# Kernel tuning notes

Measured on AMD Instinct MI355X. Metric: run time of the kernel, lower is better.

## Reference

```python
import jax, jax.numpy as jnp
import numpy as np

B, T, D = 8, 2048, 1024


def setup_inputs() -> dict:
    key = jax.random.key(0)
    ks = jax.random.split(key, 9)
    s = 1.0 / np.sqrt(D)
    return {
        "e": jax.random.normal(ks[0], (B, T, D), jnp.float32),
        "residual": jax.random.normal(ks[1], (B, T, D), jnp.float32),
        "Wq_w": jax.random.normal(ks[2], (D, D), jnp.float32) * s,
        "Wq_b": jax.random.normal(ks[3], (D,), jnp.float32) * s,
        "Wk_w": jax.random.normal(ks[4], (D, D), jnp.float32) * s,
        "Wk_b": jax.random.normal(ks[5], (D,), jnp.float32) * s,
        "Wv_w": jax.random.normal(ks[6], (D, D), jnp.float32) * s,
        "Wv_b": jax.random.normal(ks[7], (D,), jnp.float32) * s,
        "v_table": jax.random.normal(ks[8], (T, 1), jnp.float32),
    }


def reference(e, residual, Wq_w, Wq_b, Wk_w, Wk_b, Wv_w, Wv_b, v_table):
    T_ = e.shape[1]
    # relative position index: pos[i,j] = max(i - j, 0)
    pos = jnp.arange(T_)
    rel = jnp.maximum(pos[:, None] - pos[None, :], 0)          # (T, T) int
    pos_embd = v_table[rel, 0]                                 # (T, T) gather from Embedding(length, 1)

    # torch Linear: x @ W.T + b
    Q = e @ Wq_w.T + Wq_b                                      # (B, T, D)
    K = residual @ Wk_w.T + Wk_b                               # (B, T, D)
    V = e @ Wv_w.T + Wv_b                                      # (B, T, D)

    # Q @ K^T  (torch: Q @ Wk(residual).transpose(-2,-1))
    scores = jnp.einsum('btd,bsd->bts', Q, K)                  # (B, T, T)
    # einsum('BeT,Tt->BTt', K^T, pos_embd) == sum_e K[B,T,e] * pos_embd[T,t]
    scores = scores + K.sum(-1)[:, :, None] * pos_embd[None]   # (B, T, T)

    # causal mask via tril (zeros strictly-upper entries); NO softmax in this variant
    scores = scores * jnp.tril(jnp.ones((T_, T_), scores.dtype))
    return scores @ V                                          # (B, T, D)
```

## Files before the change

kernel.cpp:

```cpp
#include <hip/hip_runtime.h>

typedef unsigned short u16;
typedef __attribute__((ext_vector_type(8))) short bf16x8;
typedef __attribute__((ext_vector_type(8))) unsigned short u16x8;
typedef __attribute__((ext_vector_type(4))) float f32x4;

static __device__ __forceinline__ u16 f2bf(float f) {
  unsigned u = __float_as_uint(f);
  u += 0x7FFFu + ((u >> 16) & 1u);
  return (u16)(u >> 16);
}
static __device__ __forceinline__ float bf2f(u16 h) {
  return __uint_as_float(((unsigned)h) << 16);
}

__global__ __launch_bounds__(256) void conv_big(const float* __restrict__ e,
                                                const float* __restrict__ res,
                                                u16* __restrict__ eb, u16* __restrict__ rb) {
  int i = blockIdx.x * 256 + threadIdx.x;
  const float* in = blockIdx.z ? res : e;
  u16* out = blockIdx.z ? rb : eb;
  const float4* p = (const float4*)in + (size_t)i * 2;
  float4 a = p[0], b = p[1];
  u16x8 r;
  r[0] = f2bf(a.x); r[1] = f2bf(a.y); r[2] = f2bf(a.z); r[3] = f2bf(a.w);
  r[4] = f2bf(b.x); r[5] = f2bf(b.y); r[6] = f2bf(b.z); r[7] = f2bf(b.w);
  ((u16x8*)out)[i] = r;
}
__global__ __launch_bounds__(256) void conv_w(const float* __restrict__ w0,
                                              const float* __restrict__ w1,
                                              const float* __restrict__ w2,
                                              u16* __restrict__ o0, u16* __restrict__ o1,
                                              u16* __restrict__ o2) {
  int i = blockIdx.x * 256 + threadIdx.x;
  const float* in = blockIdx.z == 0 ? w0 : (blockIdx.z == 1 ? w1 : w2);
  u16* out = blockIdx.z == 0 ? o0 : (blockIdx.z == 1 ? o1 : o2);
  const float4* p = (const float4*)in + (size_t)i * 2;
  float4 a = p[0], b = p[1];
  u16x8 r;
  r[0] = f2bf(a.x); r[1] = f2bf(a.y); r[2] = f2bf(a.z); r[3] = f2bf(a.w);
  r[4] = f2bf(b.x); r[5] = f2bf(b.y); r[6] = f2bf(b.z); r[7] = f2bf(b.w);
  ((u16x8*)out)[i] = r;
}

__global__ __launch_bounds__(256) void ksum_kernel(const u16* __restrict__ K,
                                                   float* __restrict__ out) {
  int row = blockIdx.x * 4 + (threadIdx.x >> 6);
  int lane = threadIdx.x & 63;
  const u16x8* p = (const u16x8*)(K + (size_t)row * 1024);
  float s = 0.f;
#pragma unroll
  for (int it = 0; it < 2; ++it) {
    u16x8 v = p[lane + it * 64];
#pragma unroll
    for (int j = 0; j < 8; ++j) s += bf2f(v[j]);
  }
#pragma unroll
  for (int off = 32; off >= 1; off >>= 1) s += __shfl_down(s, off);
  if (lane == 0) out[row] = s;
}

enum { M_BIASN = 0, M_BIASM = 1, M_SCORES = 2, M_OUT = 3 };

template <int MODE, int SWZ>
static __device__ __forceinline__ void core256x128(
    const u16* __restrict__ Ab, int lda, const u16* __restrict__ Bb, int ldb,
    char* smem, int m0, int n0, int nk, void* __restrict__ Cbase, int ldc,
    const float* __restrict__ bias, const float* __restrict__ ksb,
    const float* __restrict__ vtab) {
  const int tid = threadIdx.x;
  const int lane = tid & 63;
  const int wid = tid >> 6;
  const int wm = wid >> 1, wn = wid & 1;

  char* As = smem;
  char* Bs = smem + 32768;

  const int r7 = (tid >> 3) & 7;
  const int cb = (tid & 7) << 4;
  const int gcol = SWZ ? (cb ^ (r7 << 4)) : cb;
  const int rbase_st = tid >> 3;

  const int aoff = (wm * 64 + (lane & 15)) * 128;
  const int boff = (wn * 64 + (lane & 15)) * 128;
  const int swz7 = SWZ ? (lane & 7) : 0;
  const int c0 = ((0 * 4 + (lane >> 4)) ^ swz7) << 4;
  const int c1 = ((1 * 4 + (lane >> 4)) ^ swz7) << 4;

  f32x4 acc[4][4];
#pragma unroll
  for (int m = 0; m < 4; ++m)
#pragma unroll
    for (int n = 0; n < 4; ++n) acc[m][n] = (f32x4){0.f, 0.f, 0.f, 0.f};

  for (int kt = 0; kt < nk; ++kt) {
    const int k0 = kt * 64;
#pragma unroll
    for (int i = 0; i < 4; ++i) {
      const char* ga = (const char*)(Ab + (size_t)(m0 + i * 64 + rbase_st) * lda + k0) + gcol;
      __builtin_amdgcn_global_load_lds(
          (const __attribute__((address_space(1))) void*)ga,
          (__attribute__((address_space(3))) void*)(As + i * 8192 + wid * 1024), 16, 0, 0);
    }
#pragma unroll
    for (int j = 0; j < 2; ++j) {
      const char* gb = (const char*)(Bb + (size_t)(n0 + j * 64 + rbase_st) * ldb + k0) + gcol;
      __builtin_amdgcn_global_load_lds(
          (const __attribute__((address_space(1))) void*)gb,
          (__attribute__((address_space(3))) void*)(Bs + j * 8192 + wid * 1024), 16, 0, 0);
    }
    __syncthreads();
#pragma unroll
    for (int ks = 0; ks < 2; ++ks) {
      const int cks = ks ? c1 : c0;
      bf16x8 af[4], bfv[4];
#pragma unroll
      for (int m = 0; m < 4; ++m) af[m] = *(const bf16x8*)(As + aoff + m * 2048 + cks);
#pragma unroll
      for (int n = 0; n < 4; ++n) bfv[n] = *(const bf16x8*)(Bs + boff + n * 2048 + cks);
#pragma unroll
      for (int m = 0; m < 4; ++m)
#pragma unroll
        for (int n = 0; n < 4; ++n)
          acc[m][n] = __builtin_amdgcn_mfma_f32_16x16x32_bf16(af[m], bfv[n], acc[m][n], 0, 0, 0);
    }
    __syncthreads();
  }

  u16* C16 = (u16*)Cbase;
  float* Cf = (float*)Cbase;
#pragma unroll
  for (int m = 0; m < 4; ++m) {
#pragma unroll
    for (int n = 0; n < 4; ++n) {
      const int rb = m0 + wm * 64 + m * 16 + ((lane >> 4) << 2);
      const int c = n0 + wn * 64 + n * 16 + (lane & 15);
#pragma unroll
      for (int j = 0; j < 4; ++j) {
        const int r = rb + j;
        float v = acc[m][n][j];
        if (MODE == M_BIASN) {
          v += bias[c];
          C16[(size_t)r * ldc + c] = f2bf(v);
        } else if (MODE == M_BIASM) {
          v += bias[r];
          C16[(size_t)r * ldc + c] = f2bf(v);
        } else if (MODE == M_SCORES) {
          if (c <= r) v += ksb[r] * vtab[r - c];
          else v = 0.f;
          C16[(size_t)r * ldc + c] = f2bf(v);
        } else {
          Cf[(size_t)r * ldc + c] = v;
        }
      }
    }
  }
}

template <int MODE, int SWZ>
static __device__ __forceinline__ void rect_gemm(
    const u16* A, int lda, long long sA, const u16* B, int ldb, long long sB,
    void* Cv, int ldc, long long sC, int k_len, const float* bias) {
  const int nl = gridDim.x * gridDim.y;
  const int l = blockIdx.x + gridDim.x * blockIdx.y;
  const int q8 = nl >> 3;
  const int logical = (l & 7) * q8 + (l >> 3);
  const int gx = logical % gridDim.x;
  const int gy = logical / gridDim.x;
  const int z = blockIdx.z;
  __shared__ char smem[49152];
  core256x128<MODE, SWZ>(A + (size_t)z * sA, lda, B + (size_t)z * sB, ldb, smem,
                         gy * 256, gx * 128, k_len >> 6,
                         (char*)Cv + 0, ldc, bias, nullptr, nullptr);
}

__global__ __launch_bounds__(512, 4) void k_q_proj(
    const u16* A, const u16* B, u16* C, const float* bias) {
  const int nl = gridDim.x * gridDim.y;
  const int l = blockIdx.x + gridDim.x * blockIdx.y;
  const int logical = (l & 7) * (nl >> 3) + (l >> 3);
  const int gx = logical % gridDim.x, gy = logical / gridDim.x;
  __shared__ char smem[49152];
  core256x128<M_BIASN, 0>(A, 1024, B, 1024, smem, gy * 256, gx * 128, 16,
                          C, 1024, bias, nullptr, nullptr);
}
__global__ __launch_bounds__(512, 4) void k_k_proj(
    const u16* A, const u16* B, u16* C, const float* bias) {
  const int nl = gridDim.x * gridDim.y;
  const int l = blockIdx.x + gridDim.x * blockIdx.y;
  const int logical = (l & 7) * (nl >> 3) + (l >> 3);
  const int gx = logical % gridDim.x, gy = logical / gridDim.x;
  __shared__ char smem[49152];
  core256x128<M_BIASN, 1>(A, 1024, B, 1024, smem, gy * 256, gx * 128, 16,
                          C, 1024, bias, nullptr, nullptr);
}
__global__ __launch_bounds__(512, 4) void k_v_proj(
    const u16* A, const u16* B, u16* C, const float* bias) {
  const int nl = gridDim.x * gridDim.y;
  const int l = blockIdx.x + gridDim.x * blockIdx.y;
  const int logical = (l & 7) * (nl >> 3) + (l >> 3);
  const int gx = logical % gridDim.x, gy = logical / gridDim.x;
  __shared__ char smem[49152];
  core256x128<M_BIASM, 1>(A, 1024, B, 1024, smem, gy * 256, gx * 128, 16,
                          C, 16384, bias, nullptr, nullptr);
}
__global__ __launch_bounds__(512, 4) void k_scores(
    const u16* Q, const u16* K, u16* S, const float* ksum, const float* vtab) {
  const int h = (blockIdx.x & 7) * 9 + (blockIdx.x >> 3);
  int gy = 0;
#pragma unroll
  for (int q = 1; q < 8; ++q) if (q * q + q <= h) gy = q;
  const int gx = h - (gy * gy + gy);
  const int z = blockIdx.z;
  __shared__ char smem[49152];
  core256x128<M_SCORES, 1>(Q + (size_t)z * 2048 * 1024, 1024,
                           K + (size_t)z * 2048 * 1024, 1024, smem,
                           gy * 256, gx * 128, 16,
                           S + (size_t)z * 2048 * 2048, 2048,
                           nullptr, ksum + (size_t)z * 2048, vtab);
}
__global__ __launch_bounds__(512, 4) void k_out(
    const u16* S, const u16* VT, float* O) {
  const int nl = gridDim.x * gridDim.y;
  const int l = blockIdx.x + gridDim.x * blockIdx.y;
  const int logical = (l & 7) * (nl >> 3) + (l >> 3);
  const int gx = logical % gridDim.x;
  const int p = logical / gridDim.x;
  const int z = blockIdx.z;
  __shared__ char smem[49152];
#pragma unroll
  for (int sub = 0; sub < 2; ++sub) {
    const int gy = sub ? 7 - p : p;
    const int nk = (gy + 1) * 4;
    core256x128<M_OUT, 1>(S + (size_t)z * 2048 * 2048, 2048,
                          VT + (size_t)z * 2048, 16384, smem,
                          gy * 256, gx * 128, nk,
                          O + (size_t)z * 2048 * 1024, 1024,
                          nullptr, nullptr, nullptr);
    if (sub == 0) __syncthreads();
  }
}

extern "C" void kernel_launch(void* const* d_in, const int* in_sizes, int n_in,
                              void* d_out, int out_size, void* d_ws, size_t ws_size,
                              hipStream_t stream) {
  (void)in_sizes; (void)n_in; (void)out_size; (void)ws_size;
  const float* e    = (const float*)d_in[0];
  const float* res  = (const float*)d_in[1];
  const float* Wq_w = (const float*)d_in[2];
  const float* Wq_b = (const float*)d_in[3];
  const float* Wk_w = (const float*)d_in[4];
  const float* Wk_b = (const float*)d_in[5];
  const float* Wv_w = (const float*)d_in[6];
  const float* Wv_b = (const float*)d_in[7];
  const float* vtab = (const float*)d_in[8];

  char* ws = (char*)d_ws;
  const size_t SZ = 33554432;
  u16* ebf = (u16*)(ws);
  u16* rbf = (u16*)(ws + SZ);
  u16* Qb  = (u16*)(ws + 2 * SZ);
  u16* Kb  = (u16*)(ws + 3 * SZ);
  u16* VT  = (u16*)(ws + 4 * SZ);
  u16* Wqb = (u16*)(ws + 5 * SZ);
  u16* Wkb = (u16*)(ws + 5 * SZ + 2097152);
  u16* Wvb = (u16*)(ws + 5 * SZ + 2 * 2097152);
  float* ksum = (float*)(ws + 5 * SZ + 3 * 2097152);
  u16* scores = (u16*)(ws);

  conv_big<<<dim3(8192, 1, 2), 256, 0, stream>>>(e, res, ebf, rbf);
  conv_w<<<dim3(512, 1, 3), 256, 0, stream>>>(Wq_w, Wk_w, Wv_w, Wqb, Wkb, Wvb);

  k_q_proj<<<dim3(8, 64, 1), 512, 0, stream>>>(ebf, Wqb, Qb, Wq_b);
  k_k_proj<<<dim3(8, 64, 1), 512, 0, stream>>>(rbf, Wkb, Kb, Wk_b);
  k_v_proj<<<dim3(128, 4, 1), 512, 0, stream>>>(Wvb, ebf, VT, Wv_b);

  ksum_kernel<<<4096, 256, 0, stream>>>(Kb, ksum);

  k_scores<<<dim3(72, 1, 8), 512, 0, stream>>>(Qb, Kb, scores, ksum, vtab);

  k_out<<<dim3(8, 4, 8), 512, 0, stream>>>(scores, VT, (float*)d_out);
}
```

Baseline: 304.4 us.

## Switch GEMMs from 256x128 to 128x128 tiles and merge Q/K projections

Replaces the 256x128 block tile (512 threads) with a 128x128 tile (256 threads) and less LDS for all GEMM kernels, and updates the triangular scheduling for scores and output to the finer 16x16 block grid. The Q and K projections are merged into one launch using the z grid dimension. The aim is finer causal-triangle granularity, so fewer masked-out tiles are computed, plus more blocks for occupancy and load balance. In exchange, data reuse per tile drops and global/LDS traffic per FLOP rises.

```diff
diff --git a/kernel.cpp b/kernel.cpp
--- a/kernel.cpp
+++ b/kernel.cpp
@@ -62,8 +62,8 @@
 
 enum { M_BIASN = 0, M_BIASM = 1, M_SCORES = 2, M_OUT = 3 };
 
-template <int MODE, int SWZ>
-static __device__ __forceinline__ void core256x128(
+template <int MODE>
+static __device__ __forceinline__ void core128(
     const u16* __restrict__ Ab, int lda, const u16* __restrict__ Bb, int ldb,
     char* smem, int m0, int n0, int nk, void* __restrict__ Cbase, int ldc,
     const float* __restrict__ bias, const float* __restrict__ ksb,
@@ -74,18 +74,15 @@
   const int wm = wid >> 1, wn = wid & 1;
 
   char* As = smem;
-  char* Bs = smem + 32768;
-
-  const int r7 = (tid >> 3) & 7;
-  const int cb = (tid & 7) << 4;
-  const int gcol = SWZ ? (cb ^ (r7 << 4)) : cb;
+  char* Bs = smem + 16384;
+
   const int rbase_st = tid >> 3;
+  const int gcol = ((tid & 7) << 4) ^ ((rbase_st & 7) << 4);
 
   const int aoff = (wm * 64 + (lane & 15)) * 128;
   const int boff = (wn * 64 + (lane & 15)) * 128;
-  const int swz7 = SWZ ? (lane & 7) : 0;
-  const int c0 = ((0 * 4 + (lane >> 4)) ^ swz7) << 4;
-  const int c1 = ((1 * 4 + (lane >> 4)) ^ swz7) << 4;
+  const int c0 = ((0 * 4 + (lane >> 4)) ^ (lane & 7)) << 4;
+  const int c1 = ((1 * 4 + (lane >> 4)) ^ (lane & 7)) << 4;
 
   f32x4 acc[4][4];
 #pragma unroll
@@ -97,17 +94,17 @@
     const int k0 = kt * 64;
 #pragma unroll
     for (int i = 0; i < 4; ++i) {
-      const char* ga = (const char*)(Ab + (size_t)(m0 + i * 64 + rbase_st) * lda + k0) + gcol;
+      const char* ga = (const char*)(Ab + (size_t)(m0 + i * 32 + rbase_st) * lda + k0) + gcol;
       __builtin_amdgcn_global_load_lds(
           (const __attribute__((address_space(1))) void*)ga,
-          (__attribute__((address_space(3))) void*)(As + i * 8192 + wid * 1024), 16, 0, 0);
-    }
-#pragma unroll
-    for (int j = 0; j < 2; ++j) {
-      const char* gb = (const char*)(Bb + (size_t)(n0 + j * 64 + rbase_st) * ldb + k0) + gcol;
+          (__attribute__((address_space(3))) void*)(As + i * 4096 + wid * 1024), 16, 0, 0);
+    }
+#pragma unroll
+    for (int i = 0; i < 4; ++i) {
+      const char* gb = (const char*)(Bb + (size_t)(n0 + i * 32 + rbase_st) * ldb + k0) + gcol;
       __builtin_amdgcn_global_load_lds(
           (const __attribute__((address_space(1))) void*)gb,
-          (__attribute__((address_space(3))) void*)(Bs + j * 8192 + wid * 1024), 16, 0, 0);
+          (__attribute__((address_space(3))) void*)(Bs + i * 4096 + wid * 1024), 16, 0, 0);
     }
     __syncthreads();
 #pragma unroll
@@ -157,86 +154,64 @@
   }
 }
 
-template <int MODE, int SWZ>
-static __device__ __forceinline__ void rect_gemm(
-    const u16* A, int lda, long long sA, const u16* B, int ldb, long long sB,
-    void* Cv, int ldc, long long sC, int k_len, const float* bias) {
-  const int nl = gridDim.x * gridDim.y;
-  const int l = blockIdx.x + gridDim.x * blockIdx.y;
-  const int q8 = nl >> 3;
-  const int logical = (l & 7) * q8 + (l >> 3);
-  const int gx = logical % gridDim.x;
-  const int gy = logical / gridDim.x;
-  const int z = blockIdx.z;
-  __shared__ char smem[49152];
-  core256x128<MODE, SWZ>(A + (size_t)z * sA, lda, B + (size_t)z * sB, ldb, smem,
-                         gy * 256, gx * 128, k_len >> 6,
-                         (char*)Cv + 0, ldc, bias, nullptr, nullptr);
-}
-
-__global__ __launch_bounds__(512, 4) void k_q_proj(
-    const u16* A, const u16* B, u16* C, const float* bias) {
+static __device__ __forceinline__ int2 xcd_swz_xy() {
   const int nl = gridDim.x * gridDim.y;
   const int l = blockIdx.x + gridDim.x * blockIdx.y;
   const int logical = (l & 7) * (nl >> 3) + (l >> 3);
-  const int gx = logical % gridDim.x, gy = logical / gridDim.x;
-  __shared__ char smem[49152];
-  core256x128<M_BIASN, 0>(A, 1024, B, 1024, smem, gy * 256, gx * 128, 16,
-                          C, 1024, bias, nullptr, nullptr);
-}
-__global__ __launch_bounds__(512, 4) void k_k_proj(
-    const u16* A, const u16* B, u16* C, const float* bias) {
-  const int nl = gridDim.x * gridDim.y;
-  const int l = blockIdx.x + gridDim.x * blockIdx.y;
-  const int logical = (l & 7) * (nl >> 3) + (l >> 3);
-  const int gx = logical % gridDim.x, gy = logical / gridDim.x;
-  __shared__ char smem[49152];
-  core256x128<M_BIASN, 1>(A, 1024, B, 1024, smem, gy * 256, gx * 128, 16,
-                          C, 1024, bias, nullptr, nullptr);
-}
-__global__ __launch_bounds__(512, 4) void k_v_proj(
-    const u16* A, const u16* B, u16* C, const float* bias) {
-  const int nl = gridDim.x * gridDim.y;
-  const int l = blockIdx.x + gridDim.x * blockIdx.y;
-  const int logical = (l & 7) * (nl >> 3) + (l >> 3);
-  const int gx = logical % gridDim.x, gy = logical / gridDim.x;
-  __shared__ char smem[49152];
-  core256x128<M_BIASM, 1>(A, 1024, B, 1024, smem, gy * 256, gx * 128, 16,
-                          C, 16384, bias, nullptr, nullptr);
-}
-__global__ __launch_bounds__(512, 4) void k_scores(
+  return make_int2(logical % gridDim.x, logical / gridDim.x);
+}
+
+__global__ __launch_bounds__(256, 3) void k_qk_proj(
+    const u16* eb, const u16* rb, const u16* Wq, const u16* Wk,
+    const float* bq, const float* bk, u16* Q, u16* K) {
+  int2 g = xcd_swz_xy();
+  const int zz = blockIdx.z;
+  const u16* A = zz ? rb : eb;
+  const u16* B = zz ? Wk : Wq;
+  const float* bias = zz ? bk : bq;
+  u16* C = zz ? K : Q;
+  __shared__ char smem[32768];
+  core128<M_BIASN>(A, 1024, B, 1024, smem, g.y * 128, g.x * 128, 16,
+                   C, 1024, bias, nullptr, nullptr);
+}
+__global__ __launch_bounds__(256, 3) void k_v_proj(
+    const u16* Wv, const u16* eb, u16* VT, const float* bv) {
+  int2 g = xcd_swz_xy();
+  __shared__ char smem[32768];
+  core128<M_BIASM>(Wv, 1024, eb, 1024, smem, g.y * 128, g.x * 128, 16,
+                   VT, 16384, bv, nullptr, nullptr);
+}
+__global__ __launch_bounds__(256, 3) void k_scores(
     const u16* Q, const u16* K, u16* S, const float* ksum, const float* vtab) {
-  const int h = (blockIdx.x & 7) * 9 + (blockIdx.x >> 3);
+  const int h = (blockIdx.x & 7) * 17 + (blockIdx.x >> 3);
   int gy = 0;
 #pragma unroll
-  for (int q = 1; q < 8; ++q) if (q * q + q <= h) gy = q;
-  const int gx = h - (gy * gy + gy);
+  for (int q = 1; q < 16; ++q) if (q * (q + 1) / 2 <= h) gy = q;
+  const int gx = h - gy * (gy + 1) / 2;
   const int z = blockIdx.z;
-  __shared__ char smem[49152];
-  core256x128<M_SCORES, 1>(Q + (size_t)z * 2048 * 1024, 1024,
-                           K + (size_t)z * 2048 * 1024, 1024, smem,
-                           gy * 256, gx * 128, 16,
-                           S + (size_t)z * 2048 * 2048, 2048,
-                           nullptr, ksum + (size_t)z * 2048, vtab);
-}
-__global__ __launch_bounds__(512, 4) void k_out(
+  __shared__ char smem[32768];
+  core128<M_SCORES>(Q + (size_t)z * 2048 * 1024, 1024,
+                    K + (size_t)z * 2048 * 1024, 1024, smem,
+                    gy * 128, gx * 128, 16,
+                    S + (size_t)z * 2048 * 2048, 2048,
+                    nullptr, ksum + (size_t)z * 2048, vtab);
+}
+__global__ __launch_bounds__(256, 3) void k_out(
     const u16* S, const u16* VT, float* O) {
-  const int nl = gridDim.x * gridDim.y;
-  const int l = blockIdx.x + gridDim.x * blockIdx.y;
-  const int logical = (l & 7) * (nl >> 3) + (l >> 3);
-  const int gx = logical % gridDim.x;
-  const int p = logical / gridDim.x;
+  int2 g = xcd_swz_xy();
+  const int gx = g.x;
+  const int p = g.y;
   const int z = blockIdx.z;
-  __shared__ char smem[49152];
+  __shared__ char smem[32768];
 #pragma unroll
   for (int sub = 0; sub < 2; ++sub) {
-    const int gy = sub ? 7 - p : p;
-    const int nk = (gy + 1) * 4;
-    core256x128<M_OUT, 1>(S + (size_t)z * 2048 * 2048, 2048,
-                          VT + (size_t)z * 2048, 16384, smem,
-                          gy * 256, gx * 128, nk,
-                          O + (size_t)z * 2048 * 1024, 1024,
-                          nullptr, nullptr, nullptr);
+    const int gy = sub ? 15 - p : p;
+    const int nk = (gy + 1) * 2;
+    core128<M_OUT>(S + (size_t)z * 2048 * 2048, 2048,
+                   VT + (size_t)z * 2048, 16384, smem,
+                   gy * 128, gx * 128, nk,
+                   O + (size_t)z * 2048 * 1024, 1024,
+                   nullptr, nullptr, nullptr);
     if (sub == 0) __syncthreads();
   }
 }
@@ -271,13 +246,12 @@
   conv_big<<<dim3(8192, 1, 2), 256, 0, stream>>>(e, res, ebf, rbf);
   conv_w<<<dim3(512, 1, 3), 256, 0, stream>>>(Wq_w, Wk_w, Wv_w, Wqb, Wkb, Wvb);
 
-  k_q_proj<<<dim3(8, 64, 1), 512, 0, stream>>>(ebf, Wqb, Qb, Wq_b);
-  k_k_proj<<<dim3(8, 64, 1), 512, 0, stream>>>(rbf, Wkb, Kb, Wk_b);
-  k_v_proj<<<dim3(128, 4, 1), 512, 0, stream>>>(Wvb, ebf, VT, Wv_b);
+  k_qk_proj<<<dim3(8, 128, 2), 256, 0, stream>>>(ebf, rbf, Wqb, Wkb, Wq_b, Wk_b, Qb, Kb);
+  k_v_proj<<<dim3(128, 8, 1), 256, 0, stream>>>(Wvb, ebf, VT, Wv_b);
 
   ksum_kernel<<<4096, 256, 0, stream>>>(Kb, ksum);
 
-  k_scores<<<dim3(72, 1, 8), 512, 0, stream>>>(Qb, Kb, scores, ksum, vtab);
-
-  k_out<<<dim3(8, 4, 8), 512, 0, stream>>>(scores, VT, (float*)d_out);
-}
+  k_scores<<<dim3(136, 1, 8), 256, 0, stream>>>(Qb, Kb, scores, ksum, vtab);
+
+  k_out<<<dim3(8, 8, 8), 256, 0, stream>>>(scores, VT, (float*)d_out);
+}
```

Measured after the change: 292.4 us. 3.9% less time.
